# Kernel optimization log

Hardware: AMD Instinct MI355X
Metric: run time of the kernel (lower is better)

The kernel has to match this reference:

```python
import jax, jax.numpy as jnp
import numpy as np

B, T = 256, 32
V, E, H = 10000, 512, 512


def setup_inputs() -> dict:
    key = jax.random.key(0)
    ks = jax.random.split(key, 9)
    s = 0.05
    return {
        "caps": jax.random.randint(ks[0], (B, T), 0, V),
        "latent": jax.random.normal(ks[1], (B, H), dtype=jnp.float32),
        "embed": jax.random.normal(ks[2], (V, E), dtype=jnp.float32) * s,
        "W_ih": jax.random.normal(ks[3], (4 * H, E), dtype=jnp.float32) * s,
        "W_hh": jax.random.normal(ks[4], (4 * H, H), dtype=jnp.float32) * s,
        "b_ih": jax.random.normal(ks[5], (4 * H,), dtype=jnp.float32) * s,
        "b_hh": jax.random.normal(ks[6], (4 * H,), dtype=jnp.float32) * s,
        "W_lin": jax.random.normal(ks[7], (V, H), dtype=jnp.float32) * s,
        "b_lin": jax.random.normal(ks[8], (V,), dtype=jnp.float32) * s,
    }


def reference(caps, latent, embed, W_ih, W_hh, b_ih, b_hh, W_lin, b_lin):
    # Teacher-forced decoder (train_bool=True): step i consumes caps[:, i-1],
    # writes logits into outputs[i]; outputs[0] stays zero.
    bias = b_ih + b_hh  # [4H]

    def step(carry, tok):
        h, c = carry  # [B,H] each
        x = embed[tok]  # [B,E]
        gates = x @ W_ih.T + h @ W_hh.T + bias  # [B,4H], PyTorch gate order i,f,g,o
        i_g, f_g, g_g, o_g = jnp.split(gates, 4, axis=-1)
        c = jax.nn.sigmoid(f_g) * c + jax.nn.sigmoid(i_g) * jnp.tanh(g_g)
        h = jax.nn.sigmoid(o_g) * jnp.tanh(c)
        logits = h @ W_lin.T + b_lin  # [B,V]
        return (h, c), logits

    h0 = latent
    c0 = jnp.zeros_like(latent)
    tokens = caps[:, :-1].T  # [T-1, B]: inputs for steps 1..T-1
    _, outs = jax.lax.scan(step, (h0, c0), tokens)  # [T-1, B, V]
    zero_row = jnp.zeros((1,) + outs.shape[1:], dtype=outs.dtype)
    return jnp.concatenate([zero_row, outs], axis=0)  # [T, B, V]
```

## Files before the change

### kernel.cpp

```cpp
#include <hip/hip_runtime.h>
#include <hip/hip_bf16.h>
#include <stdint.h>

#define B_    256
#define T_    32
#define V_    10000
#define E_    512
#define H_    512
#define NSTEP 31
#define M_    7936
#define NG_   2048
#define VPAD_ 10240

#define NCHAIN   64
#define NXG      248
#define XG_BASE  NCHAIN
#define LG_BASE  (NCHAIN + NXG)
#define NLOGIT   (NSTEP * 40)

typedef __attribute__((ext_vector_type(8))) short  short8;
typedef __attribute__((ext_vector_type(4))) float  f32x4;

static __device__ __forceinline__ unsigned short f2bf(float f) {
  __hip_bfloat16 h = __float2bfloat16(f);
  return *reinterpret_cast<unsigned short*>(&h);
}
static __device__ __forceinline__ ushort4 f4_to_bf4(float4 a) {
  ushort4 r; r.x = f2bf(a.x); r.y = f2bf(a.y); r.z = f2bf(a.z); r.w = f2bf(a.w); return r;
}
static __device__ __forceinline__ float fsig(float x) {
  return 1.f / (1.f + __expf(-x));
}
static __device__ __forceinline__ float ftanh_(float x) {
  x = fminf(fmaxf(x, -30.f), 30.f);
  float e = __expf(-2.f * x);
  return (1.f - e) / (1.f + e);
}

#define GLOAD_LDS16(gp, lp)                                                                   \
  __builtin_amdgcn_global_load_lds((const __attribute__((address_space(1))) unsigned int*)(gp), \
                                   (__attribute__((address_space(3))) unsigned int*)(lp), 16, 0, 0)

static __device__ __forceinline__ void store8_cc(void* p, uint2 v) {
  asm volatile("global_store_dwordx2 %0, %1, off sc0 sc1" :: "v"(p), "v"(v) : "memory");
}
static __device__ __forceinline__ void storef_cc(float* p, float v) {
  asm volatile("global_store_dword %0, %1, off sc0 sc1" :: "v"(p), "v"(v) : "memory");
}

__global__ __launch_bounds__(256) void k_init(
    const int* __restrict__ caps, const float* __restrict__ embed,
    const float* __restrict__ latent,
    const float* __restrict__ Wih, const float* __restrict__ Whh,
    const float* __restrict__ Wlin, const float* __restrict__ bih,
    const float* __restrict__ bhh,
    unsigned short* __restrict__ Wihb, unsigned short* __restrict__ Whhb,
    unsigned short* __restrict__ Wlb, float* __restrict__ bias,
    unsigned short* __restrict__ Xbf, unsigned short* __restrict__ HsAll,
    float* __restrict__ out0, int* __restrict__ cntbuf) {
  const int stride = gridDim.x * 256;
  const int i0 = blockIdx.x * 256 + threadIdx.x;
  for (int q = i0; q < (NG_ * E_) / 4; q += stride) {
    ((ushort4*)Wihb)[q] = f4_to_bf4(((const float4*)Wih)[q]);
    ((ushort4*)Whhb)[q] = f4_to_bf4(((const float4*)Whh)[q]);
  }
  for (int q = i0; q < (VPAD_ * H_) / 4; q += stride) {
    int row = q >> 7;
    ushort4 r;
    if (row < V_) r = f4_to_bf4(((const float4*)Wlin)[q]);
    else { r.x = 0; r.y = 0; r.z = 0; r.w = 0; }
    ((ushort4*)Wlb)[q] = r;
  }
  for (int q = i0; q < NG_; q += stride) bias[q] = bih[q] + bhh[q];
  for (int q = i0; q < (M_ * E_) / 4; q += stride) {
    int m = q >> 7;
    int e4 = q & 127;
    int t = m >> 8, b = m & 255;
    int tok = caps[b * T_ + t];
    float4 a = ((const float4*)(embed + (size_t)tok * E_))[e4];
    ((ushort4*)Xbf)[q] = f4_to_bf4(a);
  }
  for (int q = i0; q < (B_ * H_) / 4; q += stride)
    ((ushort4*)HsAll)[q] = f4_to_bf4(((const float4*)latent)[q]);
  float4 z = make_float4(0.f, 0.f, 0.f, 0.f);
  for (int q = i0; q < (B_ * V_) / 4; q += stride)
    ((float4*)out0)[q] = z;
  if (i0 < 256 + 32)
    cntbuf[i0] = 0;
}

__global__ __launch_bounds__(512, 2) void k_mix(
    const unsigned short* __restrict__ Xbf,
    const unsigned short* __restrict__ Wihb,
    const float* __restrict__ bias,
    float* __restrict__ Xg,
    const unsigned short* __restrict__ Whhb,
    const unsigned short* __restrict__ Wlb,
    const float* __restrict__ blin,
    unsigned short* __restrict__ HsAll,
    int* __restrict__ cnt,
    int* __restrict__ xcnt,
    float* __restrict__ out) {
  __shared__ uint4 smem_raw[131072 / 16];
  const int tid = threadIdx.x;
  const int w = tid >> 6, l = tid & 63;
  const int lr = l & 15;

  if (blockIdx.x < NCHAIN) {
    unsigned short* hsh = (unsigned short*)smem_raw;
    float* gsh = (float*)((char*)smem_raw + 32768);
    const int gb = blockIdx.x & 7;
    const int ct = blockIdx.x >> 3;
    const int b0 = gb << 5;
    const int n0 = ct << 6;
    const int g  = w >> 1;
    const int cs = (w & 1) << 5;
    const int lk = (l >> 4) << 3;

    short8 bf0[16], bf1[16];
    {
      const unsigned short* wb0 = Whhb + (size_t)(g * 512 + n0 + cs + lr) * 512 + lk;
      const unsigned short* wb1 = wb0 + (size_t)16 * 512;
#pragma unroll 16
      for (int ks = 0; ks < 16; ++ks) {
        bf0[ks] = *(const short8*)(wb0 + (ks << 5));
        bf1[ks] = *(const short8*)(wb1 + (ks << 5));
      }
    }
    float c_reg[4] = {0.f, 0.f, 0.f, 0.f};
    const int br  = tid >> 4;
    const int nc0 = (tid & 15) << 2;
    const size_t xg_base = ((size_t)(b0 + br) << 11) + n0 + nc0;

    for (int t = 0; t < NSTEP; ++t) {
      {
        int ok;
        do {
          int val = 1;
          if (tid == 0)
            val = (__hip_atomic_load(&xcnt[t], __ATOMIC_RELAXED,
                                     __HIP_MEMORY_SCOPE_AGENT) == 8);
          else if (tid == 64 && t > 0)
            val = (__hip_atomic_load(&cnt[t * 8 + gb], __ATOMIC_RELAXED,
                                     __HIP_MEMORY_SCOPE_AGENT) == 8);
          ok = __syncthreads_and(val);
          if (!ok) __builtin_amdgcn_s_sleep(2);
        } while (!ok);
      }

#pragma unroll
      for (int j = 0; j < 4; ++j) {
        int row = (j << 3) + w;
        const unsigned short* gsrc = HsAll + (size_t)t * B_ * H_ +
                                     (size_t)(b0 + row) * 512 + ((l ^ (row & 7)) << 3);
        GLOAD_LDS16(gsrc, hsh + row * 512);
      }
      const f32x4* xp = (const f32x4*)(Xg + (size_t)t * B_ * NG_ + xg_base);
      f32x4 xiv = xp[0], xfv = xp[128], xgv = xp[256], xov = xp[384];
      __syncthreads();

      f32x4 acc[2][2] = {};
#pragma unroll
      for (int ks = 0; ks < 16; ++ks) {
        int kc = (ks << 2) + (l >> 4);
        short8 a0 = *(const short8*)(hsh + lr * 512 + ((kc ^ (lr & 7)) << 3));
        short8 a1 = *(const short8*)(hsh + (16 + lr) * 512 + ((kc ^ (lr & 7)) << 3));
        acc[0][0] = __builtin_amdgcn_mfma_f32_16x16x32_bf16(a0, bf0[ks], acc[0][0], 0, 0, 0);
        acc[0][1] = __builtin_amdgcn_mfma_f32_16x16x32_bf16(a0, bf1[ks], acc[0][1], 0, 0, 0);
        acc[1][0] = __builtin_amdgcn_mfma_f32_16x16x32_bf16(a1, bf0[ks], acc[1][0], 0, 0, 0);
        acc[1][1] = __builtin_amdgcn_mfma_f32_16x16x32_bf16(a1, bf1[ks], acc[1][1], 0, 0, 0);
      }

      const int gr0 = (l >> 4) << 2;
#pragma unroll
      for (int m = 0; m < 2; ++m)
#pragma unroll
        for (int n = 0; n < 2; ++n)
#pragma unroll
          for (int r = 0; r < 4; ++r)
            gsh[g * 2048 + (m * 16 + gr0 + r) * 64 + cs + n * 16 + lr] = acc[m][n][r];
      __syncthreads();

      f32x4 giv = *(const f32x4*)&gsh[0 * 2048 + br * 64 + nc0];
      f32x4 gfv = *(const f32x4*)&gsh[1 * 2048 + br * 64 + nc0];
      f32x4 ggv = *(const f32x4*)&gsh[2 * 2048 + br * 64 + nc0];
      f32x4 gov = *(const f32x4*)&gsh[3 * 2048 + br * 64 + nc0];
      ushort4 hv; unsigned short* hvp = &hv.x;
#pragma unroll
      for (int j = 0; j < 4; ++j) {
        float is = fsig(giv[j] + xiv[j]);
        float fs = fsig(gfv[j] + xfv[j]);
        float os = fsig(gov[j] + xov[j]);
        float gt = ftanh_(ggv[j] + xgv[j]);
        float cn = fs * c_reg[j] + is * gt;
        c_reg[j] = cn;
        hvp[j] = f2bf(os * ftanh_(cn));
      }
      unsigned short* h_out = HsAll + (size_t)(t + 1) * B_ * H_;
      store8_cc(h_out + ((size_t)(b0 + br) << 9) + n0 + nc0,
                *reinterpret_cast<uint2*>(&hv));

      asm volatile("s_waitcnt vmcnt(0)" ::: "memory");
      __syncthreads();
      if (tid == 0)
        __hip_atomic_fetch_add(&cnt[(t + 1) * 8 + gb], 1, __ATOMIC_RELAXED,
                               __HIP_MEMORY_SCOPE_AGENT);
    }
  } else if (blockIdx.x < LG_BASE) {
    unsigned short* As = (unsigned short*)smem_raw;
    unsigned short* Bs = (unsigned short*)((char*)smem_raw + 65536);
    const int idx = blockIdx.x - XG_BASE;
    const int bm = idx >> 3;
    const int bn = idx & 7;
    const int wr = w >> 2, wc = w & 3;
    const int srow = (w << 3) + (l >> 3);
    const int schunk = (l & 7) ^ ((l >> 3) & 7);
    const unsigned short* Ab = Xbf + (size_t)(bm * 256 + srow) * 512 + (schunk << 3);
    const unsigned short* Bb = Wihb + (size_t)(bn * 256 + srow) * 512 + (schunk << 3);
    unsigned short* Al = As + (w << 9);
    unsigned short* Bl = Bs + (w << 9);

    f32x4 acc[8][4] = {};
#pragma unroll
    for (int i = 0; i < 4; ++i) {
      GLOAD_LDS16(Ab + (size_t)(i << 6) * 512, Al + (i << 12));
      GLOAD_LDS16(Bb + (size_t)(i << 6) * 512, Bl + (i << 12));
    }
    asm volatile("s_waitcnt vmcnt(0)" ::: "memory");
    __syncthreads();

    for (int kt = 0; kt < 8; ++kt) {
      const int cur = (kt & 1) << 14;
      if (kt < 7) {
        const int nb = ((kt & 1) ^ 1) << 14;
        const int k0 = (kt + 1) << 6;
#pragma unroll
        for (int i = 0; i < 4; ++i) {
          GLOAD_LDS16(Ab + (size_t)(i << 6) * 512 + k0, Al + nb + (i << 12));
          GLOAD_LDS16(Bb + (size_t)(i << 6) * 512 + k0, Bl + nb + (i << 12));
        }
      }
      const unsigned short* ab = As + cur;
      const unsigned short* bb = Bs + cur;
#pragma unroll
      for (int kc = 0; kc < 2; ++kc) {
        const int cI = (kc << 2) + (l >> 4);
        const int rchunk = (cI ^ (lr & 7)) << 3;
        short8 af[8], bf8[4];
#pragma unroll
        for (int m = 0; m < 8; ++m)
          af[m] = *(const short8*)(ab + ((wr << 7) + (m << 4) + lr) * 64 + rchunk);
#pragma unroll
        for (int n = 0; n < 4; ++n)
          bf8[n] = *(const short8*)(bb + ((wc << 6) + (n << 4) + lr) * 64 + rchunk);
#pragma unroll
        for (int m = 0; m < 8; ++m)
#pragma unroll
          for (int n = 0; n < 4; ++n)
            acc[m][n] = __builtin_amdgcn_mfma_f32_16x16x32_bf16(af[m], bf8[n], acc[m][n], 0, 0, 0);
      }
      asm volatile("s_waitcnt vmcnt(0)" ::: "memory");
      __syncthreads();
    }

    const int orow0 = bm * 256 + (wr << 7) + ((l >> 4) << 2);
    const int ocol0 = bn * 256 + (wc << 6) + lr;
#pragma unroll
    for (int n = 0; n < 4; ++n) {
      int col = ocol0 + (n << 4);
      float bv = bias[col];
#pragma unroll
      for (int m = 0; m < 8; ++m) {
        int row = orow0 + (m << 4);
#pragma unroll
        for (int r = 0; r < 4; ++r)
          storef_cc(&Xg[(size_t)(row + r) * NG_ + col], acc[m][n][r] + bv);
      }
    }
    asm volatile("s_waitcnt vmcnt(0)" ::: "memory");
    __syncthreads();
    if (tid == 0)
      __hip_atomic_fetch_add(&xcnt[bm], 1, __ATOMIC_RELAXED,
                             __HIP_MEMORY_SCOPE_AGENT);
  } else {
    unsigned short* As = (unsigned short*)smem_raw;
    unsigned short* Bs = (unsigned short*)((char*)smem_raw + 65536);
    const int idx = blockIdx.x - LG_BASE;
    const int t  = idx / 40 + 1;
    const int bn = idx % 40;

    {
      int ok;
      do {
        int val = 1;
        if (tid < 8)
          val = (__hip_atomic_load(&cnt[t * 8 + tid], __ATOMIC_RELAXED,
                                   __HIP_MEMORY_SCOPE_AGENT) == 8);
        ok = __syncthreads_and(val);
        if (!ok) __builtin_amdgcn_s_sleep(32);
      } while (!ok);
    }

    const unsigned short* slotT = HsAll + (size_t)t * B_ * H_;
    const int wr = w >> 2, wc = w & 3;
    const int srow = (w << 3) + (l >> 3);
    const int schunk = (l & 7) ^ ((l >> 3) & 7);
    const unsigned short* Ab = slotT + (size_t)srow * 512 + (schunk << 3);
    const unsigned short* Bb = Wlb + (size_t)(bn * 256 + srow) * 512 + (schunk << 3);
    unsigned short* Al = As + (w << 9);
    unsigned short* Bl = Bs + (w << 9);

    f32x4 acc[8][4] = {};
#pragma unroll
    for (int i = 0; i < 4; ++i) {
      GLOAD_LDS16(Ab + (size_t)(i << 6) * 512, Al + (i << 12));
      GLOAD_LDS16(Bb + (size_t)(i << 6) * 512, Bl + (i << 12));
    }
    asm volatile("s_waitcnt vmcnt(0)" ::: "memory");
    __syncthreads();

    for (int kt = 0; kt < 8; ++kt) {
      const int cur = (kt & 1) << 14;
      if (kt < 7) {
        const int nb = ((kt & 1) ^ 1) << 14;
        const int k0 = (kt + 1) << 6;
#pragma unroll
        for (int i = 0; i < 4; ++i) {
          GLOAD_LDS16(Ab + (size_t)(i << 6) * 512 + k0, Al + nb + (i << 12));
          GLOAD_LDS16(Bb + (size_t)(i << 6) * 512 + k0, Bl + nb + (i << 12));
        }
      }
      const unsigned short* ab = As + cur;
      const unsigned short* bb = Bs + cur;
#pragma unroll
      for (int kc = 0; kc < 2; ++kc) {
        const int cI = (kc << 2) + (l >> 4);
        const int rchunk = (cI ^ (lr & 7)) << 3;
        short8 af[8], bf8[4];
#pragma unroll
        for (int m = 0; m < 8; ++m)
          af[m] = *(const short8*)(ab + ((wr << 7) + (m << 4) + lr) * 64 + rchunk);
#pragma unroll
        for (int n = 0; n < 4; ++n)
          bf8[n] = *(const short8*)(bb + ((wc << 6) + (n << 4) + lr) * 64 + rchunk);
#pragma unroll
        for (int m = 0; m < 8; ++m)
#pragma unroll
          for (int n = 0; n < 4; ++n)
            acc[m][n] = __builtin_amdgcn_mfma_f32_16x16x32_bf16(af[m], bf8[n], acc[m][n], 0, 0, 0);
      }
      asm volatile("s_waitcnt vmcnt(0)" ::: "memory");
      __syncthreads();
    }

    const int orow0 = t * 256 + (wr << 7) + ((l >> 4) << 2);
    const int ocol0 = bn * 256 + (wc << 6) + lr;
#pragma unroll
    for (int n = 0; n < 4; ++n) {
      int col = ocol0 + (n << 4);
      if (col < V_) {
        float bv = blin[col];
#pragma unroll
        for (int m = 0; m < 8; ++m) {
          int row = orow0 + (m << 4);
#pragma unroll
          for (int r = 0; r < 4; ++r)
            __builtin_nontemporal_store(acc[m][n][r] + bv,
                &out[(size_t)(row + r) * V_ + col]);
        }
      }
    }
  }
}

extern "C" void kernel_launch(void* const* d_in, const int* in_sizes, int n_in,
                              void* d_out, int out_size, void* d_ws, size_t ws_size,
                              hipStream_t stream) {
  const int*   caps   = (const int*)d_in[0];
  const float* latent = (const float*)d_in[1];
  const float* embed  = (const float*)d_in[2];
  const float* Wih    = (const float*)d_in[3];
  const float* Whh    = (const float*)d_in[4];
  const float* bih    = (const float*)d_in[5];
  const float* bhh    = (const float*)d_in[6];
  const float* Wlin   = (const float*)d_in[7];
  const float* blin   = (const float*)d_in[8];
  float* out = (float*)d_out;

  char* ws = (char*)d_ws;
  size_t off = 0;
  auto alloc = [&](size_t bytes) {
    void* p = ws + off;
    off = (off + bytes + 255) & ~(size_t)255;
    return p;
  };
  unsigned short* Xbf   = (unsigned short*)alloc((size_t)M_ * E_ * 2);
  unsigned short* Wihb  = (unsigned short*)alloc((size_t)NG_ * E_ * 2);
  unsigned short* Whhb  = (unsigned short*)alloc((size_t)NG_ * H_ * 2);
  unsigned short* Wlb   = (unsigned short*)alloc((size_t)VPAD_ * H_ * 2);
  float*          bias  = (float*)alloc((size_t)NG_ * 4);
  float*          Xg    = (float*)alloc((size_t)M_ * NG_ * 4);
  unsigned short* HsAll = (unsigned short*)alloc((size_t)(NSTEP + 1) * B_ * H_ * 2);
  int*            cntb  = (int*)alloc((size_t)(256 + 32) * 4);
  int* cnt  = cntb;
  int* xcnt = cntb + 256;
  (void)ws_size; (void)in_sizes; (void)n_in; (void)out_size;

  hipLaunchKernelGGL(k_init, dim3(2048), dim3(256), 0, stream,
                     caps, embed, latent, Wih, Whh, Wlin, bih, bhh,
                     Wihb, Whhb, Wlb, bias, Xbf, HsAll, out, cntb);
  hipLaunchKernelGGL(k_mix, dim3(NCHAIN + NXG + NLOGIT), dim3(512), 0, stream,
                     Xbf, Wihb, bias, Xg, Whhb, Wlb, blin, HsAll, cnt, xcnt, out);
}
```

Baseline: 226.5 us.

## Replace per-step counter barrier with sentinel-polled hidden-state handoff

The recurrent chain blocks now detect that the previous step's hidden state is ready by polling the state buffer for a NaN sentinel pattern, written into all future steps during init. This removes the per-step store drain, block barrier and counter atomic from the critical path. The ready counter for step t is now bumped only after a block has actually read h_t, and once more at the end for the final step. The Xg producer uses plain stores plus a release atomic instead of cache-bypassing stores. The cost is an extra sentinel fill pass in init and a spin loop that reloads the state, and correctness now depends on real hidden values never matching the sentinel bit pattern.

```diff
diff --git a/kernel.cpp b/kernel.cpp
--- a/kernel.cpp
+++ b/kernel.cpp
@@ -11,6 +11,7 @@
 #define M_    7936
 #define NG_   2048
 #define VPAD_ 10240
+#define SENTU 0x7FC07FC0u
 
 #define NCHAIN   64
 #define NXG      248
@@ -44,8 +45,10 @@
 static __device__ __forceinline__ void store8_cc(void* p, uint2 v) {
   asm volatile("global_store_dwordx2 %0, %1, off sc0 sc1" :: "v"(p), "v"(v) : "memory");
 }
-static __device__ __forceinline__ void storef_cc(float* p, float v) {
-  asm volatile("global_store_dword %0, %1, off sc0 sc1" :: "v"(p), "v"(v) : "memory");
+static __device__ __forceinline__ uint4 load16_cc(const void* p) {
+  uint4 r;
+  asm volatile("global_load_dwordx4 %0, %1, off sc0 sc1" : "=v"(r) : "v"(p) : "memory");
+  return r;
 }
 
 __global__ __launch_bounds__(256) void k_init(
@@ -82,6 +85,10 @@
   }
   for (int q = i0; q < (B_ * H_) / 4; q += stride)
     ((ushort4*)HsAll)[q] = f4_to_bf4(((const float4*)latent)[q]);
+  uint4 s4 = make_uint4(SENTU, SENTU, SENTU, SENTU);
+  uint4* hs1 = (uint4*)(HsAll + (size_t)B_ * H_);
+  for (int q = i0; q < (NSTEP * B_ * H_) / 8; q += stride)
+    hs1[q] = s4;
   float4 z = make_float4(0.f, 0.f, 0.f, 0.f);
   for (int q = i0; q < (B_ * V_) / 4; q += stride)
     ((float4*)out0)[q] = z;
@@ -129,7 +136,8 @@
     }
     float c_reg[4] = {0.f, 0.f, 0.f, 0.f};
     const int br  = tid >> 4;
-    const int nc0 = (tid & 15) << 2;
+    const int ch  = tid & 15;
+    const int nc0 = ch << 2;
     const size_t xg_base = ((size_t)(b0 + br) << 11) + n0 + nc0;
 
     for (int t = 0; t < NSTEP; ++t) {
@@ -140,23 +148,41 @@
           if (tid == 0)
             val = (__hip_atomic_load(&xcnt[t], __ATOMIC_RELAXED,
                                      __HIP_MEMORY_SCOPE_AGENT) == 8);
-          else if (tid == 64 && t > 0)
-            val = (__hip_atomic_load(&cnt[t * 8 + gb], __ATOMIC_RELAXED,
-                                     __HIP_MEMORY_SCOPE_AGENT) == 8);
           ok = __syncthreads_and(val);
           if (!ok) __builtin_amdgcn_s_sleep(2);
         } while (!ok);
       }
-
-#pragma unroll
-      for (int j = 0; j < 4; ++j) {
-        int row = (j << 3) + w;
-        const unsigned short* gsrc = HsAll + (size_t)t * B_ * H_ +
-                                     (size_t)(b0 + row) * 512 + ((l ^ (row & 7)) << 3);
-        GLOAD_LDS16(gsrc, hsh + row * 512);
-      }
       const f32x4* xp = (const f32x4*)(Xg + (size_t)t * B_ * NG_ + xg_base);
       f32x4 xiv = xp[0], xfv = xp[128], xgv = xp[256], xov = xp[384];
+
+      const unsigned short* h_in = HsAll + (size_t)t * B_ * H_ +
+                                   (size_t)(b0 + br) * 512;
+      uint4 hreg[4];
+      int ok;
+      do {
+#pragma unroll
+        for (int j = 0; j < 4; ++j)
+          hreg[j] = load16_cc(h_in + ((ch + (j << 4)) << 3));
+        asm volatile("s_waitcnt vmcnt(0)" ::: "memory");
+        __builtin_amdgcn_sched_barrier(0);
+        int val = 1;
+#pragma unroll
+        for (int j = 0; j < 4; ++j) {
+          val &= (hreg[j].x != SENTU); val &= (hreg[j].y != SENTU);
+          val &= (hreg[j].z != SENTU); val &= (hreg[j].w != SENTU);
+        }
+        ok = __syncthreads_and(val);
+        if (!ok) __builtin_amdgcn_s_sleep(1);
+      } while (!ok);
+      if (tid == 0 && t >= 1)
+        __hip_atomic_fetch_add(&cnt[t * 8 + gb], 1, __ATOMIC_RELAXED,
+                               __HIP_MEMORY_SCOPE_AGENT);
+
+#pragma unroll
+      for (int j = 0; j < 4; ++j) {
+        int cj = ch + (j << 4);
+        *(uint4*)(hsh + br * 512 + ((cj ^ (br & 7)) << 3)) = hreg[j];
+      }
       __syncthreads();
 
       f32x4 acc[2][2] = {};
@@ -199,13 +225,12 @@
       unsigned short* h_out = HsAll + (size_t)(t + 1) * B_ * H_;
       store8_cc(h_out + ((size_t)(b0 + br) << 9) + n0 + nc0,
                 *reinterpret_cast<uint2*>(&hv));
-
-      asm volatile("s_waitcnt vmcnt(0)" ::: "memory");
-      __syncthreads();
-      if (tid == 0)
-        __hip_atomic_fetch_add(&cnt[(t + 1) * 8 + gb], 1, __ATOMIC_RELAXED,
-                               __HIP_MEMORY_SCOPE_AGENT);
-    }
+    }
+    asm volatile("s_waitcnt vmcnt(0)" ::: "memory");
+    __syncthreads();
+    if (tid == 0)
+      __hip_atomic_fetch_add(&cnt[NSTEP * 8 + gb], 1, __ATOMIC_RELAXED,
+                             __HIP_MEMORY_SCOPE_AGENT);
   } else if (blockIdx.x < LG_BASE) {
     unsigned short* As = (unsigned short*)smem_raw;
     unsigned short* Bs = (unsigned short*)((char*)smem_raw + 65536);
@@ -274,13 +299,13 @@
         int row = orow0 + (m << 4);
 #pragma unroll
         for (int r = 0; r < 4; ++r)
-          storef_cc(&Xg[(size_t)(row + r) * NG_ + col], acc[m][n][r] + bv);
+          Xg[(size_t)(row + r) * NG_ + col] = acc[m][n][r] + bv;
       }
     }
     asm volatile("s_waitcnt vmcnt(0)" ::: "memory");
     __syncthreads();
     if (tid == 0)
-      __hip_atomic_fetch_add(&xcnt[bm], 1, __ATOMIC_RELAXED,
+      __hip_atomic_fetch_add(&xcnt[bm], 1, __ATOMIC_RELEASE,
                              __HIP_MEMORY_SCOPE_AGENT);
   } else {
     unsigned short* As = (unsigned short*)smem_raw;
```

New measurement: 214.6 us, median of 2. -5.3%, faster.
